# Kernel tuning notes

Measured on AMD Instinct MI355X. Metric: run time of the kernel, lower is better.

The kernel has to match this reference:

```python
import jax, jax.numpy as jnp
import numpy as np

B, T, D, H, W = 2, 8192, 512, 8, 256
d = D // H  # 64
NC = T // W  # number of chunks (T divisible by W)


def setup_inputs() -> dict:
    key = jax.random.key(0)
    ks = jax.random.split(key, 9)
    s = 1.0 / np.sqrt(D).astype(np.float32)
    x = jax.random.normal(ks[0], (B, T, D), jnp.float32)
    Wq = jax.random.normal(ks[1], (D, D), jnp.float32) * s
    Wk = jax.random.normal(ks[2], (D, D), jnp.float32) * s
    Wv = jax.random.normal(ks[3], (D, D), jnp.float32) * s
    Wo = jax.random.normal(ks[4], (D, D), jnp.float32) * s
    bq = jax.random.normal(ks[5], (D,), jnp.float32) * 0.01
    bk = jax.random.normal(ks[6], (D,), jnp.float32) * 0.01
    bv = jax.random.normal(ks[7], (D,), jnp.float32) * 0.01
    bo = jax.random.normal(ks[8], (D,), jnp.float32) * 0.01
    return {"x": x, "Wq": Wq, "bq": bq, "Wk": Wk, "bk": bk,
            "Wv": Wv, "bv": bv, "Wo": Wo, "bo": bo}


def _local_attention(q, k, v):
    # q, k, v: [B, H, T, d]. Each W-sized query chunk attends to keys in
    # [chunk_start - W, chunk_end + W) -> a 3W window, masked at boundaries.
    qc = q.reshape(B, H, NC, W, d)
    pad = ((0, 0), (0, 0), (W, W), (0, 0))
    kp = jnp.pad(k, pad)
    vp = jnp.pad(v, pad)
    # window gather indices into padded sequence: [NC, 3W]
    pos = jnp.arange(NC)[:, None] * W + jnp.arange(3 * W)[None, :]
    kw = kp[:, :, pos, :]  # [B, H, NC, 3W, d]
    vw = vp[:, :, pos, :]  # [B, H, NC, 3W, d]
    valid = (pos >= W) & (pos < T + W)  # [NC, 3W] true for real (unpadded) keys
    scores = jnp.einsum('bhcqd,bhckd->bhcqk', qc, kw) * (d ** -0.5)
    scores = jnp.where(valid[None, None, :, None, :], scores, -jnp.inf)
    attn = jax.nn.softmax(scores, axis=-1)
    out = jnp.einsum('bhcqk,bhckd->bhcqd', attn, vw)
    return out.reshape(B, H, T, d)


def reference(x, Wq, bq, Wk, bk, Wv, bv, Wo, bo):
    # Linear = x @ W.T + b (torch nn.Linear convention)
    q = (x @ Wq.T + bq).reshape(B, T, H, d).transpose(0, 2, 1, 3)
    # k_proj / v_proj run under torch.no_grad() in the original
    k = jax.lax.stop_gradient(x @ Wk.T + bk).reshape(B, T, H, d).transpose(0, 2, 1, 3)
    v = jax.lax.stop_gradient(x @ Wv.T + bv).reshape(B, T, H, d).transpose(0, 2, 1, 3)
    out = _local_attention(q, k, v)           # [B, H, T, d]
    out = out.transpose(0, 2, 1, 3).reshape(B, T, D)
    return out @ Wo.T + bo
```

## Files before the change

kernel.cpp:

```cpp
#include <hip/hip_runtime.h>
#include <hip/hip_bf16.h>

typedef unsigned short u16;
typedef unsigned int   u32;
typedef __bf16 bf16x8 __attribute__((ext_vector_type(8)));
typedef float  f32x4  __attribute__((ext_vector_type(4)));

#define BB 2
#define TT 8192
#define DD 512
#define HH 8
#define WW 256
#define DH 64
#define NX 8388608
#define NW 262144

__device__ __forceinline__ float b2f(u16 u) {
    unsigned int x = ((unsigned int)u) << 16;
    return __builtin_bit_cast(float, x);
}
__device__ __forceinline__ u16 f2b(float f) {
    __bf16 h = (__bf16)f;
    return __builtin_bit_cast(u16, h);
}
__device__ __forceinline__ bf16x8 ldsfrag(const u16* p) {
    return *(const bf16x8*)p;
}
__device__ __forceinline__ f32x4 mfma16(bf16x8 a, bf16x8 b, f32x4 c) {
    return __builtin_amdgcn_mfma_f32_16x16x32_bf16(a, b, c, 0, 0, 0);
}

typedef __attribute__((address_space(1))) u32 gu32;
typedef __attribute__((address_space(3))) u32 lu32;
__device__ __forceinline__ void gl_lds(const u16* g, u16* l) {
    __builtin_amdgcn_global_load_lds((gu32*)g, (lu32*)l, 16, 0, 0);
}

__device__ __forceinline__ void cvt8(const void* s, u16* d, long i, int f) {
    if (f) {
        const u32* sp = (const u32*)s + i;
        uint4 a = *(const uint4*)(sp);
        uint4 b = *(const uint4*)(sp + 4);
        u16 o[8];
        o[0] = f2b(__builtin_bit_cast(float, a.x));
        o[1] = f2b(__builtin_bit_cast(float, a.y));
        o[2] = f2b(__builtin_bit_cast(float, a.z));
        o[3] = f2b(__builtin_bit_cast(float, a.w));
        o[4] = f2b(__builtin_bit_cast(float, b.x));
        o[5] = f2b(__builtin_bit_cast(float, b.y));
        o[6] = f2b(__builtin_bit_cast(float, b.z));
        o[7] = f2b(__builtin_bit_cast(float, b.w));
        *(uint4*)(d + i) = *(const uint4*)o;
    } else {
        *(uint4*)(d + i) = *(const uint4*)((const u16*)s + i);
    }
}

__global__ void convert_all(const void* x, const void* Wq, const void* bq,
                            const void* Wk, const void* bk, const void* Wv,
                            const void* bv, const void* Wo, const void* bo,
                            u16* __restrict__ xb, u16* __restrict__ Wcat,
                            u16* __restrict__ Wob, u16* __restrict__ bcat,
                            u16* __restrict__ bob, int* __restrict__ flagw)
{
    __shared__ int sflag;
    const int tid = threadIdx.x;
    if (tid == 0) sflag = 0;
    __syncthreads();
    int mybad = 0;
    for (int i = tid; i < 2048; i += 256) {
        float v = b2f(((const u16*)x)[i]);
        if (!(fabsf(v) < 100.f)) mybad = 1;
    }
    if (mybad) atomicOr(&sflag, 1);
    __syncthreads();
    const int f = sflag ? 1 : 0;
    if (blockIdx.x == 0 && tid == 0) *flagw = f;

    long i = ((long)blockIdx.x * 256 + tid) * 8;
    if (i < NX)            { cvt8(x,  xb,           i, f); return; }
    i -= NX;
    if (i < NW)            { cvt8(Wq, Wcat,         i, f); return; }
    i -= NW;
    if (i < NW)            { cvt8(Wk, Wcat + NW,    i, f); return; }
    i -= NW;
    if (i < NW)            { cvt8(Wv, Wcat + 2*NW,  i, f); return; }
    i -= NW;
    if (i < NW)            { cvt8(Wo, Wob,          i, f); return; }
    i -= NW;
    if (i < 512)           { cvt8(bq, bcat,         i, f); return; }
    i -= 512;
    if (i < 512)           { cvt8(bk, bcat + 512,   i, f); return; }
    i -= 512;
    if (i < 512)           { cvt8(bv, bcat + 1024,  i, f); return; }
    i -= 512;
    if (i < 512)           { cvt8(bo, bob,          i, f); }
}

__global__ __launch_bounds__(512, 2)
void gemm256(const u16* __restrict__ A, const u16* __restrict__ Bw,
             const u16* __restrict__ bias, void* __restrict__ out0,
             u16* __restrict__ out1, u16* __restrict__ out2,
             int mode, const int* __restrict__ flagp)
{
    __shared__ __align__(16) u16 AsF[3][256 * 64];
    __shared__ __align__(16) u16 BsF[3][128 * 64];

    const int tid  = threadIdx.x;
    const int lane = tid & 63;
    const int wv   = tid >> 6;
    const int col  = lane & 15;
    const int quad = lane >> 4;
    const int wm   = (wv >> 1) * 64;
    const int wn   = (wv & 1) * 64;
    const int m0   = blockIdx.x * 256;
    const int n0   = blockIdx.y * 128;

    f32x4 acc[4][4] = {};

    const int lr  = lane >> 3;
    const int lc  = lane & 7;
    const int cbs = lc ^ lr;

    auto STG = [&](int buf, int k0, int half) {
        #pragma unroll
        for (int i = 0; i < 2; i++) {
            const int g = wv * 4 + half * 2 + i;
            gl_lds(A + (size_t)(m0 + g * 8 + lr) * 512 + k0 + cbs * 8,
                   &AsF[buf][g * 512]);
        }
        const int g2 = wv * 2 + half;
        gl_lds(Bw + (size_t)(n0 + g2 * 8 + lr) * 512 + k0 + cbs * 8,
               &BsF[buf][g2 * 512]);
    };

    STG(0, 0, 0);  STG(0, 0, 1);
    STG(1, 64, 0); STG(1, 64, 1);
    asm volatile("s_waitcnt vmcnt(6)" ::: "memory");
    __builtin_amdgcn_s_barrier();
    __builtin_amdgcn_sched_barrier(0);

    #pragma unroll
    for (int t = 0; t < 8; t++) {
        const int p  = t % 3;
        const int q  = (t + 2) % 3;
        const int k2 = (t + 2) * 64;
        bf16x8 fa[2][4], fb[2][4];
        #pragma unroll
        for (int mi = 0; mi < 4; mi++)
            fa[0][mi] = ldsfrag(&AsF[p][(wm + mi * 16 + col) * 64 + ((0 + quad) ^ (col & 7)) * 8]);
        #pragma unroll
        for (int ni = 0; ni < 4; ni++)
            fb[0][ni] = ldsfrag(&BsF[p][(wn + ni * 16 + col) * 64 + ((0 + quad) ^ (col & 7)) * 8]);
        if (t < 6) STG(q, k2, 0);
        #pragma unroll
        for (int mi = 0; mi < 4; mi++)
            fa[1][mi] = ldsfrag(&AsF[p][(wm + mi * 16 + col) * 64 + ((4 + quad) ^ (col & 7)) * 8]);
        #pragma unroll
        for (int ni = 0; ni < 4; ni++)
            fb[1][ni] = ldsfrag(&BsF[p][(wn + ni * 16 + col) * 64 + ((4 + quad) ^ (col & 7)) * 8]);
        if (t < 6) STG(q, k2, 1);
        asm volatile("s_waitcnt lgkmcnt(0)" ::: "memory");
        __builtin_amdgcn_sched_barrier(0);
        __builtin_amdgcn_s_setprio(1);
        #pragma unroll
        for (int kk = 0; kk < 2; kk++)
            #pragma unroll
            for (int mi = 0; mi < 4; mi++)
                #pragma unroll
                for (int ni = 0; ni < 4; ni++)
                    acc[mi][ni] = mfma16(fa[kk][mi], fb[kk][ni], acc[mi][ni]);
        __builtin_amdgcn_s_setprio(0);
        if (t < 6)      asm volatile("s_waitcnt vmcnt(6)" ::: "memory");
        else if (t == 6) asm volatile("s_waitcnt vmcnt(0)" ::: "memory");
        if (t < 7) {
            __builtin_amdgcn_s_barrier();
            __builtin_amdgcn_sched_barrier(0);
        }
    }

    if (mode == 0) {
        #pragma unroll
        for (int ni = 0; ni < 4; ni++) {
            const int gn = n0 + wn + ni * 16 + col;
            const float bv = b2f(bias[gn]);
            const int seg = gn >> 9;
            const float sc = (seg == 0) ? 0.125f : 1.0f;
            #pragma unroll
            for (int mi = 0; mi < 4; mi++) {
                const int gmb = m0 + wm + mi * 16 + quad * 4;
                if (seg < 2) {
                    u16* dst = (seg == 0) ? (u16*)out0 : out1;
                    #pragma unroll
                    for (int r = 0; r < 4; r++)
                        dst[(size_t)(gmb + r) * 512 + (gn & 511)] = f2b((acc[mi][ni][r] + bv) * sc);
                } else {
                    const int d = gn & 63, hh = (gn >> 6) & 7;
                    const int bb = gmb >> 13, t = gmb & 8191;
                    u16 pb[4];
                    #pragma unroll
                    for (int r = 0; r < 4; r++) pb[r] = f2b(acc[mi][ni][r] + bv);
                    uint2 pk;
                    pk.x = pb[0] | ((u32)pb[1] << 16);
                    pk.y = pb[2] | ((u32)pb[3] << 16);
                    *(uint2*)&out2[((size_t)(bb * 8 + hh) * 64 + d) * 8192 + t] = pk;
                }
            }
        }
    } else {
        const int outf32 = *flagp;
        #pragma unroll
        for (int ni = 0; ni < 4; ni++) {
            const int gn = n0 + wn + ni * 16 + col;
            const float bv = b2f(bias[gn]);
            #pragma unroll
            for (int mi = 0; mi < 4; mi++) {
                #pragma unroll
                for (int r = 0; r < 4; r++) {
                    const int gm = m0 + wm + mi * 16 + quad * 4 + r;
                    const float v = acc[mi][ni][r] + bv;
                    if (outf32) ((float*)out0)[(size_t)gm * 512 + gn] = v;
                    else        ((u16*)out0)[(size_t)gm * 512 + gn]  = f2b(v);
                }
            }
        }
    }
}

__global__ __launch_bounds__(512, 4)
void attn_local(const u16* __restrict__ Qg, const u16* __restrict__ Kg,
                const u16* __restrict__ VTg, u16* __restrict__ Og)
{
    __shared__ __align__(16) u16 Ks[2][64 * 64];
    __shared__ __align__(16) u16 VTs[2][64 * 64];

    const int tid  = threadIdx.x;
    const int lane = tid & 63;
    const int wv   = tid >> 6;
    const int col  = lane & 15;
    const int quad = lane >> 4;

    const int idx = blockIdx.x;
    const int c = idx & 31;
    const int h = (idx >> 5) & 7;
    const int b = idx >> 8;

    const int t0 = c * WW;
    const int wq = wv * 32;

    const int sc_lo = (c == 0) ? 4 : 0;
    const int nsc   = (c == 0 || c == 31) ? 8 : 12;

    const int ldr = lane >> 3;
    const int ldc = lane & 7;

    bf16x8 qf[2][2];
    {
        const size_t qbase = ((size_t)(b * TT + t0 + wq + col)) * DD + h * DH + quad * 8;
        #pragma unroll
        for (int qi = 0; qi < 2; qi++)
            #pragma unroll
            for (int kk = 0; kk < 2; kk++)
                qf[qi][kk] = *(const bf16x8*)(Qg + qbase + (size_t)qi * 16 * DD + kk * 32);
    }

    f32x4 o[4][2] = {};
    float lsum[2] = {0.f, 0.f};

    {
        const int kstart = t0 - WW + sc_lo * 64;
        const int rr = wv * 8 + ldr;
        const int cb = ldc ^ (rr & 7);
        gl_lds(Kg  + ((size_t)(b * TT + kstart + rr)) * DD + h * DH + cb * 8,
               &Ks[0][wv * 512]);
        gl_lds(VTg + ((size_t)((b * HH + h) * DH + rr)) * TT + kstart + cb * 8,
               &VTs[0][wv * 512]);
    }

    for (int it = 0; it < nsc; it++) {
        __syncthreads();
        if (it + 1 < nsc) {
            const int kstart = t0 - WW + (sc_lo + it + 1) * 64;
            const int buf = (it + 1) & 1;
            const int rr = wv * 8 + ldr;
            const int cb = ldc ^ (rr & 7);
            gl_lds(Kg  + ((size_t)(b * TT + kstart + rr)) * DD + h * DH + cb * 8,
                   &Ks[buf][wv * 512]);
            gl_lds(VTg + ((size_t)((b * HH + h) * DH + rr)) * TT + kstart + cb * 8,
                   &VTs[buf][wv * 512]);
        }
        const u16* ks = &Ks[it & 1][0];
        const u16* vs = &VTs[it & 1][0];

        #pragma unroll
        for (int half = 0; half < 2; half++) {
            uint2 p2[2][2];
            #pragma unroll
            for (int nsl = 0; nsl < 2; nsl++) {
                const int ns = half * 2 + nsl;
                const int row = ns * 16 + col;
                bf16x8 ka0 = ldsfrag(&ks[row * 64 + ((0 + quad) ^ (col & 7)) * 8]);
                bf16x8 ka1 = ldsfrag(&ks[row * 64 + ((4 + quad) ^ (col & 7)) * 8]);
                #pragma unroll
                for (int qi = 0; qi < 2; qi++) {
                    f32x4 sv = (f32x4){0.f, 0.f, 0.f, 0.f};
                    sv = mfma16(ka0, qf[qi][0], sv);
                    sv = mfma16(ka1, qf[qi][1], sv);
                    u16 pb[4];
                    #pragma unroll
                    for (int r = 0; r < 4; r++) {
                        const float p = __expf(sv[r]);
                        pb[r] = f2b(p);
                        lsum[qi] += p;
                    }
                    p2[nsl][qi].x = pb[0] | ((u32)pb[1] << 16);
                    p2[nsl][qi].y = pb[2] | ((u32)pb[3] << 16);
                }
            }
            bf16x8 pf[2];
            #pragma unroll
            for (int qi = 0; qi < 2; qi++) {
                uint4 w;
                w.x = p2[0][qi].x; w.y = p2[0][qi].y;
                w.z = p2[1][qi].x; w.w = p2[1][qi].y;
                pf[qi] = __builtin_bit_cast(bf16x8, w);
            }
            const int glo = (half * 4 +     (quad >> 1)) ^ (col & 7);
            const int ghi = (half * 4 + 2 + (quad >> 1)) ^ (col & 7);
            const int hb  = (quad & 1) * 8;
            #pragma unroll
            for (int di = 0; di < 4; di++) {
                const char* rowp = (const char*)&vs[(di * 16 + col) * 64];
                uint2 lo = *(const uint2*)(rowp + glo * 16 + hb);
                uint2 hi = *(const uint2*)(rowp + ghi * 16 + hb);
                uint4 w4;
                w4.x = lo.x; w4.y = lo.y; w4.z = hi.x; w4.w = hi.y;
                bf16x8 va = __builtin_bit_cast(bf16x8, w4);
                #pragma unroll
                for (int qi = 0; qi < 2; qi++)
                    o[di][qi] = mfma16(va, pf[qi], o[di][qi]);
            }
        }
    }

    #pragma unroll
    for (int qi = 0; qi < 2; qi++) {
        float l = lsum[qi];
        l += __shfl_xor(l, 16);
        l += __shfl_xor(l, 32);
        lsum[qi] = 1.0f / l;
    }

    #pragma unroll
    for (int qi = 0; qi < 2; qi++) {
        const size_t ob = ((size_t)(b * TT + t0 + wq + qi * 16 + col)) * DD + h * DH + quad * 4;
        #pragma unroll
        for (int di = 0; di < 4; di++) {
            u16 pb[4];
            #pragma unroll
            for (int r = 0; r < 4; r++) pb[r] = f2b(o[di][qi][r] * lsum[qi]);
            uint2 pk;
            pk.x = pb[0] | ((u32)pb[1] << 16);
            pk.y = pb[2] | ((u32)pb[3] << 16);
            *(uint2*)&Og[ob + di * 16] = pk;
        }
    }
}

extern "C" void kernel_launch(void* const* d_in, const int* in_sizes, int n_in,
                              void* d_out, int out_size, void* d_ws, size_t ws_size,
                              hipStream_t stream)
{
    u16* ws   = (u16*)d_ws;
    u16* xb   = ws;
    u16* Wcat = xb + NX;
    u16* Wob  = Wcat + 3 * NW;
    u16* bcat = Wob + NW;
    u16* bob  = bcat + 1536;
    u16* qws  = bob + 512;
    u16* kws  = qws + NX;
    u16* vtws = kws + NX;
    u16* aws  = vtws + NX;
    int* flag = (int*)(aws + NX);

    convert_all<<<4609, 256, 0, stream>>>(
        d_in[0], d_in[1], d_in[2], d_in[3], d_in[4], d_in[5], d_in[6], d_in[7], d_in[8],
        xb, Wcat, Wob, bcat, bob, flag);

    gemm256<<<dim3(64, 12), 512, 0, stream>>>(xb, Wcat, bcat, qws, kws, vtws, 0, flag);
    attn_local<<<dim3(BB * HH * 32), 512, 0, stream>>>(qws, kws, vtws, aws);
    gemm256<<<dim3(64, 4), 512, 0, stream>>>(aws, Wob, bob, d_out, nullptr, nullptr, 1, flag);
}
```

Before: 191.2 us.

## Triple-buffer K/V tiles in local attention with explicit vmcnt waits

```diff
diff --git a/kernel.cpp b/kernel.cpp
--- a/kernel.cpp
+++ b/kernel.cpp
@@ -227,12 +227,12 @@
     }
 }
 
-__global__ __launch_bounds__(512, 4)
+__global__ __launch_bounds__(512, 3)
 void attn_local(const u16* __restrict__ Qg, const u16* __restrict__ Kg,
                 const u16* __restrict__ VTg, u16* __restrict__ Og)
 {
-    __shared__ __align__(16) u16 Ks[2][64 * 64];
-    __shared__ __align__(16) u16 VTs[2][64 * 64];
+    __shared__ __align__(16) u16 Ks[3][64 * 64];
+    __shared__ __align__(16) u16 VTs[3][64 * 64];
 
     const int tid  = threadIdx.x;
     const int lane = tid & 63;
@@ -248,8 +248,8 @@
     const int t0 = c * WW;
     const int wq = wv * 32;
 
-    const int sc_lo = (c == 0) ? 4 : 0;
-    const int nsc   = (c == 0 || c == 31) ? 8 : 12;
+    const int lo = (c == 0)  ? 4 : 0;
+    const int hi = (c == 31) ? 8 : 12;
 
     const int ldr = lane >> 3;
     const int ldc = lane & 7;
@@ -267,79 +267,86 @@
     f32x4 o[4][2] = {};
     float lsum[2] = {0.f, 0.f};
 
-    {
-        const int kstart = t0 - WW + sc_lo * 64;
+    auto STAGE = [&](int buf, int sc) {
+        int kstart = t0 - WW + sc * 64;
+        kstart = kstart < 0 ? 0 : (kstart > TT - 64 ? TT - 64 : kstart);
         const int rr = wv * 8 + ldr;
         const int cb = ldc ^ (rr & 7);
         gl_lds(Kg  + ((size_t)(b * TT + kstart + rr)) * DD + h * DH + cb * 8,
-               &Ks[0][wv * 512]);
+               &Ks[buf][wv * 512]);
         gl_lds(VTg + ((size_t)((b * HH + h) * DH + rr)) * TT + kstart + cb * 8,
-               &VTs[0][wv * 512]);
-    }
-
-    for (int it = 0; it < nsc; it++) {
-        __syncthreads();
-        if (it + 1 < nsc) {
-            const int kstart = t0 - WW + (sc_lo + it + 1) * 64;
-            const int buf = (it + 1) & 1;
-            const int rr = wv * 8 + ldr;
-            const int cb = ldc ^ (rr & 7);
-            gl_lds(Kg  + ((size_t)(b * TT + kstart + rr)) * DD + h * DH + cb * 8,
-                   &Ks[buf][wv * 512]);
-            gl_lds(VTg + ((size_t)((b * HH + h) * DH + rr)) * TT + kstart + cb * 8,
-                   &VTs[buf][wv * 512]);
-        }
-        const u16* ks = &Ks[it & 1][0];
-        const u16* vs = &VTs[it & 1][0];
-
-        #pragma unroll
-        for (int half = 0; half < 2; half++) {
-            uint2 p2[2][2];
-            #pragma unroll
-            for (int nsl = 0; nsl < 2; nsl++) {
-                const int ns = half * 2 + nsl;
-                const int row = ns * 16 + col;
-                bf16x8 ka0 = ldsfrag(&ks[row * 64 + ((0 + quad) ^ (col & 7)) * 8]);
-                bf16x8 ka1 = ldsfrag(&ks[row * 64 + ((4 + quad) ^ (col & 7)) * 8]);
+               &VTs[buf][wv * 512]);
+    };
+
+    STAGE(0, 0);
+    STAGE(1, 1);
+    asm volatile("s_waitcnt vmcnt(2)" ::: "memory");
+    __builtin_amdgcn_s_barrier();
+    __builtin_amdgcn_sched_barrier(0);
+
+    #pragma unroll
+    for (int it = 0; it < 12; it++) {
+        const int p = it % 3;
+        if (it < 10) STAGE((it + 2) % 3, it + 2);
+        if (it >= lo && it < hi) {
+            const u16* ks = &Ks[p][0];
+            const u16* vs = &VTs[p][0];
+
+            #pragma unroll
+            for (int half = 0; half < 2; half++) {
+                uint2 p2[2][2];
+                #pragma unroll
+                for (int nsl = 0; nsl < 2; nsl++) {
+                    const int ns = half * 2 + nsl;
+                    const int row = ns * 16 + col;
+                    bf16x8 ka0 = ldsfrag(&ks[row * 64 + ((0 + quad) ^ (col & 7)) * 8]);
+                    bf16x8 ka1 = ldsfrag(&ks[row * 64 + ((4 + quad) ^ (col & 7)) * 8]);
+                    #pragma unroll
+                    for (int qi = 0; qi < 2; qi++) {
+                        f32x4 sv = (f32x4){0.f, 0.f, 0.f, 0.f};
+                        sv = mfma16(ka0, qf[qi][0], sv);
+                        sv = mfma16(ka1, qf[qi][1], sv);
+                        u16 pb[4];
+                        #pragma unroll
+                        for (int r = 0; r < 4; r++) {
+                            const float p_ = __expf(sv[r]);
+                            pb[r] = f2b(p_);
+                            lsum[qi] += p_;
+                        }
+                        p2[nsl][qi].x = pb[0] | ((u32)pb[1] << 16);
+                        p2[nsl][qi].y = pb[2] | ((u32)pb[3] << 16);
+                    }
+                }
+                bf16x8 pf[2];
                 #pragma unroll
                 for (int qi = 0; qi < 2; qi++) {
-                    f32x4 sv = (f32x4){0.f, 0.f, 0.f, 0.f};
-                    sv = mfma16(ka0, qf[qi][0], sv);
-                    sv = mfma16(ka1, qf[qi][1], sv);
-                    u16 pb[4];
+                    uint4 w;
+                    w.x = p2[0][qi].x; w.y = p2[0][qi].y;
+                    w.z = p2[1][qi].x; w.w = p2[1][qi].y;
+                    pf[qi] = __builtin_bit_cast(bf16x8, w);
+                }
+                const int glo = (half * 4 +     (quad >> 1)) ^ (col & 7);
+                const int ghi = (half * 4 + 2 + (quad >> 1)) ^ (col & 7);
+                const int hb  = (quad & 1) * 8;
+                #pragma unroll
+                for (int di = 0; di < 4; di++) {
+                    const char* rowp = (const char*)&vs[(di * 16 + col) * 64];
+                    uint2 lov = *(const uint2*)(rowp + glo * 16 + hb);
+                    uint2 hiv = *(const uint2*)(rowp + ghi * 16 + hb);
+                    uint4 w4;
+                    w4.x = lov.x; w4.y = lov.y; w4.z = hiv.x; w4.w = hiv.y;
+                    bf16x8 va = __builtin_bit_cast(bf16x8, w4);
                     #pragma unroll
-                    for (int r = 0; r < 4; r++) {
-                        const float p = __expf(sv[r]);
-                        pb[r] = f2b(p);
-                        lsum[qi] += p;
-                    }
-                    p2[nsl][qi].x = pb[0] | ((u32)pb[1] << 16);
-                    p2[nsl][qi].y = pb[2] | ((u32)pb[3] << 16);
+                    for (int qi = 0; qi < 2; qi++)
+                        o[di][qi] = mfma16(va, pf[qi], o[di][qi]);
                 }
             }
-            bf16x8 pf[2];
-            #pragma unroll
-            for (int qi = 0; qi < 2; qi++) {
-                uint4 w;
-                w.x = p2[0][qi].x; w.y = p2[0][qi].y;
-                w.z = p2[1][qi].x; w.w = p2[1][qi].y;
-                pf[qi] = __builtin_bit_cast(bf16x8, w);
-            }
-            const int glo = (half * 4 +     (quad >> 1)) ^ (col & 7);
-            const int ghi = (half * 4 + 2 + (quad >> 1)) ^ (col & 7);
-            const int hb  = (quad & 1) * 8;
-            #pragma unroll
-            for (int di = 0; di < 4; di++) {
-                const char* rowp = (const char*)&vs[(di * 16 + col) * 64];
-                uint2 lo = *(const uint2*)(rowp + glo * 16 + hb);
-                uint2 hi = *(const uint2*)(rowp + ghi * 16 + hb);
-                uint4 w4;
-                w4.x = lo.x; w4.y = lo.y; w4.z = hi.x; w4.w = hi.y;
-                bf16x8 va = __builtin_bit_cast(bf16x8, w4);
-                #pragma unroll
-                for (int qi = 0; qi < 2; qi++)
-                    o[di][qi] = mfma16(va, pf[qi], o[di][qi]);
-            }
+        }
+        if (it < 10)       asm volatile("s_waitcnt vmcnt(2)" ::: "memory");
+        else if (it == 10) asm volatile("s_waitcnt vmcnt(0)" ::: "memory");
+        if (it < 11) {
+            __builtin_amdgcn_s_barrier();
+            __builtin_amdgcn_sched_barrier(0);
         }
     }
 
```

Result: slower. 196.8 us (+2.9%).
